# Performance work log

Hardware: AMD Instinct MI355X
Metric: run time of the kernel (lower is better)

The kernel has to match this reference:

```python
import jax, jax.numpy as jnp
import numpy as np

TAU = 1.0
EPS = 1e-8  # torch cosine_similarity norm clamp


def setup_inputs() -> dict:
    key = jax.random.key(0)
    k1, k2, k3 = jax.random.split(key, 3)
    B, d, M, C = 4096, 128, 8192, 16
    f = jax.random.normal(k1, (B, d), dtype=jnp.float32)
    f_neg = jax.random.normal(k2, (M, d), dtype=jnp.float32)
    labels = jax.random.randint(k3, (B,), 0, C, dtype=jnp.int64)
    return {"f": f, "f_neg": f_neg, "labels": labels, "batch_size": B}


def _normalize(x):
    n = jnp.linalg.norm(x, axis=-1, keepdims=True)
    return x / jnp.maximum(n, EPS)


def reference(f, f_neg, labels, batch_size):
    B = batch_size
    fn = _normalize(f)            # [B, d]
    gn = _normalize(f_neg)        # [M, d]

    sim_bb = jnp.einsum('id,jd->ij', fn, fn)   # [B, B] cosine sims in-batch
    sim_bn = jnp.einsum('id,md->im', fn, gn)   # [B, M] sims with neg bank

    offdiag = ~jnp.eye(B, dtype=bool)                       # exclude self
    pos_mask = (labels[:, None] == labels[None, :]) & offdiag  # [B, B]

    exp_bb = jnp.exp(sim_bb / TAU) * offdiag                # self row removed
    exp_bn = jnp.exp(sim_bn / TAU)
    # denominator_i = sum over all non-self in-batch + all bank negatives
    denom = exp_bb.sum(axis=1) + exp_bn.sum(axis=1)         # [B]

    # -log(exp(s_p/tau)/denom) = log(denom) - s_p/tau, averaged over positives
    neg_log = jnp.log(denom)[:, None] - sim_bb / TAU        # [B, B]
    n_pos = pos_mask.sum(axis=1)                            # [B]
    loss_i = jnp.sum(jnp.where(pos_mask, neg_log, 0.0), axis=1) / n_pos

    return jnp.sum(loss_i) / B  # reduction='mean'
```

## Files before the change

kernel.cpp:

```cpp
#include <hip/hip_runtime.h>
#include <hip/hip_bf16.h>
#include <hip/hip_fp8.h>

#define B_ROWS 4096
#define D_K    128
#define M_ROWS 8192
#define N_TOT  12288
#define NCHUNK 32
#define JT_PER_CHUNK 6
#define JCOLS  64
#define NCLS   16

typedef __attribute__((ext_vector_type(4))) int   intx4;
typedef __attribute__((ext_vector_type(8))) int   intx8;
typedef __attribute__((ext_vector_type(4))) float floatx4;

__device__ __forceinline__ float fp8_to_f32(unsigned char b) {
    __hip_fp8_e4m3 h; h.__x = b; return float(h);
}

__global__ __launch_bounds__(256) void nrm_kernel(
    const float* __restrict__ f, const float* __restrict__ fneg,
    unsigned char* __restrict__ G8, unsigned char* __restrict__ A8,
    float* __restrict__ S, int* __restrict__ hist, float* __restrict__ out)
{
    const int tid  = threadIdx.x;
    const int wave = tid >> 6;
    const int lane = tid & 63;
    const int row  = blockIdx.x * 4 + wave;
    if (blockIdx.x == 0) {
        #pragma unroll
        for (int k = 0; k < 8; ++k) S[tid + k * 256] = 0.f;
        if (tid < NCLS) hist[tid] = 0;
        if (tid == 0) out[0] = 0.f;
    }
    const float* src = (row < B_ROWS) ? (f + (size_t)row * D_K)
                                      : (fneg + (size_t)(row - B_ROWS) * D_K);
    float2 v = *reinterpret_cast<const float2*>(src + lane * 2);
    float ss = v.x * v.x + v.y * v.y;
    #pragma unroll
    for (int m = 1; m < 64; m <<= 1) ss += __shfl_xor(ss, m, 64);
    const float scale = 1.0f / fmaxf(sqrtf(ss), 1e-8f);
    __hip_fp8_e4m3 q0(v.x * scale);
    __hip_fp8_e4m3 q1(v.y * scale);
    const unsigned short pk =
        (unsigned short)q0.__x | ((unsigned short)q1.__x << 8);
    *reinterpret_cast<unsigned short*>(G8 + (size_t)row * D_K + lane * 2) = pk;
    if (row < B_ROWS) {
        const float s2 = scale * 1.44269504f;
        __hip_fp8_e4m3 a0(v.x * s2);
        __hip_fp8_e4m3 a1(v.y * s2);
        const unsigned short pa =
            (unsigned short)a0.__x | ((unsigned short)a1.__x << 8);
        *reinterpret_cast<unsigned short*>(A8 + (size_t)row * D_K + lane * 2) = pa;
    }
}

__global__ __launch_bounds__(256, 4) void sim_kernel(
    const unsigned char* __restrict__ G8, const unsigned char* __restrict__ A8,
    const int* __restrict__ labels, float* __restrict__ part_d,
    float* __restrict__ S, int* __restrict__ hist)
{
    __shared__ unsigned char Bs[2][JCOLS * D_K];

    const int tid = threadIdx.x;

    if (blockIdx.y >= 32) {
        const int svc    = (blockIdx.y - 32) * NCHUNK + blockIdx.x;
        const int stripe = svc & 31;
        const int dc     = svc >> 5;
        float* Sp = (float*)&Bs[0][0];
        int*   lh = (int*)(Sp + NCLS * 32);
        for (int k = tid; k < NCLS * 32; k += 256) Sp[k] = 0.f;
        if (tid < NCLS) lh[tid] = 0;
        __syncthreads();

        const int j0 = stripe * 128;
        if (dc == 0 && tid < 128) atomicAdd(&lh[labels[j0 + tid]], 1);

        const int d = tid & 31;
        const int w = tid >> 5;
        for (int jj = w; jj < 128; jj += 8) {
            const int j = j0 + jj;
            const int c = labels[j];
            atomicAdd(&Sp[c * 32 + d],
                      fp8_to_f32(G8[(size_t)j * D_K + dc * 32 + d]));
        }
        __syncthreads();
        for (int k = tid; k < NCLS * 32; k += 256)
            atomicAdd(&S[(k >> 5) * D_K + dc * 32 + (k & 31)], Sp[k]);
        if (dc == 0 && tid < NCLS) atomicAdd(&hist[tid], lh[tid]);
        return;
    }

    const int jc   = blockIdx.x;
    const int it   = blockIdx.y;
    const int wave = tid >> 6;
    const int lane = tid & 63;
    const int i0   = it * 128 + wave * 32;

    const int r16 = lane & 15;
    const int grp = lane >> 4;

    const unsigned char* Abase = A8 + (size_t)(i0 + r16) * D_K + grp * 32;
    intx8 afr[2];
    #pragma unroll
    for (int a = 0; a < 2; ++a)
        afr[a] = *reinterpret_cast<const intx8*>(Abase + (size_t)a * 16 * D_K);

    float dsum[2][4];
    #pragma unroll
    for (int a = 0; a < 2; ++a)
        #pragma unroll
        for (int r = 0; r < 4; ++r) dsum[a][r] = 0.f;

    int srcoff[2];
    #pragma unroll
    for (int s = 0; s < 2; ++s) {
        const int row  = s * 32 + (tid >> 3);
        const int gran = (tid & 7) ^ (row & 7);
        srcoff[s] = row * D_K + gran * 16;
    }

    intx4 streg[2];
    {
        const unsigned char* src =
            G8 + (size_t)(jc * JT_PER_CHUNK) * JCOLS * D_K;
        #pragma unroll
        for (int s = 0; s < 2; ++s)
            streg[s] = *reinterpret_cast<const intx4*>(src + srcoff[s]);
        #pragma unroll
        for (int s = 0; s < 2; ++s)
            *reinterpret_cast<intx4*>(&Bs[0][0] + s * 4096 + tid * 16) =
                streg[s];
    }

    for (int t = 0; t < JT_PER_CHUNK; ++t) {
        const int cur = t & 1;
        __syncthreads();

        if (t + 1 < JT_PER_CHUNK) {
            const unsigned char* src =
                G8 + (size_t)(jc * JT_PER_CHUNK + t + 1) * JCOLS * D_K;
            #pragma unroll
            for (int s = 0; s < 2; ++s)
                streg[s] = *reinterpret_cast<const intx4*>(src + srcoff[s]);
        }

        floatx4 acc[2][4];
        #pragma unroll
        for (int a = 0; a < 2; ++a)
            #pragma unroll
            for (int b = 0; b < 4; ++b)
                acc[a][b] = (floatx4){0.f, 0.f, 0.f, 0.f};

        const unsigned char* base = &Bs[cur][0];
        #pragma unroll
        for (int b = 0; b < 4; ++b) {
            const int jloc = b * 16 + r16;
            const int sw   = jloc & 7;
            intx4 lo = *reinterpret_cast<const intx4*>(
                base + jloc * D_K + ((2 * grp)     ^ sw) * 16);
            intx4 hi = *reinterpret_cast<const intx4*>(
                base + jloc * D_K + ((2 * grp + 1) ^ sw) * 16);
            intx8 bfr;
            #pragma unroll
            for (int e = 0; e < 4; ++e) { bfr[e] = lo[e]; bfr[e + 4] = hi[e]; }
            #pragma unroll
            for (int a = 0; a < 2; ++a)
                acc[a][b] = __builtin_amdgcn_mfma_scale_f32_16x16x128_f8f6f4(
                    afr[a], bfr, acc[a][b], 0, 0,
                    0, 0x7F7F7F7F, 0, 0x7F7F7F7F);
        }

        #pragma unroll
        for (int a = 0; a < 2; ++a)
            #pragma unroll
            for (int r = 0; r < 4; ++r) {
                float s0 = exp2f(acc[a][0][r]) + exp2f(acc[a][1][r]);
                float s1 = exp2f(acc[a][2][r]) + exp2f(acc[a][3][r]);
                dsum[a][r] += s0 + s1;
            }

        if (t + 1 < JT_PER_CHUNK) {
            #pragma unroll
            for (int s = 0; s < 2; ++s)
                *reinterpret_cast<intx4*>(
                    &Bs[cur ^ 1][0] + s * 4096 + tid * 16) = streg[s];
        }
    }

    #pragma unroll
    for (int a = 0; a < 2; ++a)
        #pragma unroll
        for (int r = 0; r < 4; ++r) {
            #pragma unroll
            for (int m = 1; m < 16; m <<= 1)
                dsum[a][r] += __shfl_xor(dsum[a][r], m, 64);
        }
    if (r16 == 0) {
        #pragma unroll
        for (int a = 0; a < 2; ++a)
            #pragma unroll
            for (int r = 0; r < 4; ++r)
                part_d[(size_t)(i0 + a * 16 + grp * 4 + r) * NCHUNK + jc] =
                    dsum[a][r];
    }
}

__global__ __launch_bounds__(256) void fin_kernel(
    const unsigned char* __restrict__ G8, const float* __restrict__ part_d,
    const float* __restrict__ S, const int* __restrict__ labels,
    const int* __restrict__ hist, float* __restrict__ out)
{
    const int tid  = threadIdx.x;
    const int wave = tid >> 6;
    const int lane = tid & 63;

    float lsum = 0.f;
    #pragma unroll 2
    for (int rr = 0; rr < 8; ++rr) {
        const int i   = (blockIdx.x * 4 + wave) * 8 + rr;
        const int lab = labels[i];
        float pd = (lane < NCHUNK) ? part_d[(size_t)i * NCHUNK + lane] : 0.f;
        const unsigned char* gr = G8 + (size_t)i * D_K + lane * 2;
        const float f0 = fp8_to_f32(gr[0]);
        const float f1 = fp8_to_f32(gr[1]);
        float2 sv = *reinterpret_cast<const float2*>(S + lab * D_K + lane * 2);
        float self = f0 * f0 + f1 * f1;
        float sp   = f0 * sv.x + f1 * sv.y;
        #pragma unroll
        for (int m = 1; m < 64; m <<= 1) {
            pd   += __shfl_xor(pd, m, 64);
            self += __shfl_xor(self, m, 64);
            sp   += __shfl_xor(sp, m, 64);
        }
        if (lane == 0) {
            const float npos  = (float)(hist[lab] - 1);
            const float denom = pd - __expf(self);
            lsum += __logf(denom) - (sp - self) / npos;
        }
    }
    __shared__ float w4[4];
    if (lane == 0) w4[wave] = lsum;
    __syncthreads();
    if (tid == 0)
        atomicAdd(out, (w4[0] + w4[1] + w4[2] + w4[3]) * (1.0f / (float)B_ROWS));
}

extern "C" void kernel_launch(void* const* d_in, const int* in_sizes, int n_in,
                              void* d_out, int out_size, void* d_ws, size_t ws_size,
                              hipStream_t stream) {
    const float* f      = (const float*)d_in[0];
    const float* fneg   = (const float*)d_in[1];
    const int*   labels = (const int*)d_in[2];
    float*       out    = (float*)d_out;

    char* ws = (char*)d_ws;
    unsigned char* G8     = (unsigned char*)(ws);
    unsigned char* A8     = (unsigned char*)(ws + 1572864);
    float*         part_d = (float*)(ws + 1572864 + 524288);
    float*         S      = (float*)(ws + 1572864 + 524288 + 524288);
    int*           hist   = (int*)(ws + 1572864 + 524288 + 524288 + 8192);

    nrm_kernel<<<N_TOT / 4, 256, 0, stream>>>(f, fneg, G8, A8, S, hist, out);

    dim3 gridS(NCHUNK, 36);
    sim_kernel<<<gridS, 256, 0, stream>>>(G8, A8, labels, part_d, S, hist);

    fin_kernel<<<128, 256, 0, stream>>>(G8, part_d, S, labels, hist, out);
}
```

Measured before the change: 36.17 us.

## Fuse finalize pass into sim kernel via global completion counters

Removes the separate finalize kernel launch. The 128 service blocks in the sim grid first build the class sums, then spin on global atomic counters until all 1024 sim blocks and all service blocks are done, and then compute the per-row loss themselves. This saves one launch and its gap. It risks deadlock if the spinning blocks occupy slots that the sim blocks still need, although the grid likely fits on the device. The spinning blocks also hold resources and add atomic traffic.

New measurement: 76.54 us. 112% more time.

```diff
diff --git a/kernel.cpp b/kernel.cpp
--- a/kernel.cpp
+++ b/kernel.cpp
@@ -10,6 +10,8 @@
 #define JT_PER_CHUNK 6
 #define JCOLS  64
 #define NCLS   16
+#define SIM_BLOCKS 1024
+#define SVC_BLOCKS 128
 
 typedef __attribute__((ext_vector_type(4))) int   intx4;
 typedef __attribute__((ext_vector_type(8))) int   intx8;
@@ -22,7 +24,8 @@
 __global__ __launch_bounds__(256) void nrm_kernel(
     const float* __restrict__ f, const float* __restrict__ fneg,
     unsigned char* __restrict__ G8, unsigned char* __restrict__ A8,
-    float* __restrict__ S, int* __restrict__ hist, float* __restrict__ out)
+    float* __restrict__ S, int* __restrict__ hist, float* __restrict__ out,
+    int* __restrict__ cnt)
 {
     const int tid  = threadIdx.x;
     const int wave = tid >> 6;
@@ -32,7 +35,7 @@
         #pragma unroll
         for (int k = 0; k < 8; ++k) S[tid + k * 256] = 0.f;
         if (tid < NCLS) hist[tid] = 0;
-        if (tid == 0) out[0] = 0.f;
+        if (tid == 0) { out[0] = 0.f; cnt[0] = 0; cnt[1] = 0; }
     }
     const float* src = (row < B_ROWS) ? (f + (size_t)row * D_K)
                                       : (fneg + (size_t)(row - B_ROWS) * D_K);
@@ -59,11 +62,14 @@
 __global__ __launch_bounds__(256, 4) void sim_kernel(
     const unsigned char* __restrict__ G8, const unsigned char* __restrict__ A8,
     const int* __restrict__ labels, float* __restrict__ part_d,
-    float* __restrict__ S, int* __restrict__ hist)
+    float* __restrict__ S, int* __restrict__ hist, float* __restrict__ out,
+    int* __restrict__ cnt)
 {
     __shared__ unsigned char Bs[2][JCOLS * D_K];
 
-    const int tid = threadIdx.x;
+    const int tid  = threadIdx.x;
+    const int wave = tid >> 6;
+    const int lane = tid & 63;
 
     if (blockIdx.y >= 32) {
         const int svc    = (blockIdx.y - 32) * NCHUNK + blockIdx.x;
@@ -90,14 +96,54 @@
         for (int k = tid; k < NCLS * 32; k += 256)
             atomicAdd(&S[(k >> 5) * D_K + dc * 32 + (k & 31)], Sp[k]);
         if (dc == 0 && tid < NCLS) atomicAdd(&hist[tid], lh[tid]);
+
+        __syncthreads();
+        if (tid == 0) {
+            __threadfence();
+            atomicAdd(&cnt[1], 1);
+            while (atomicAdd(&cnt[0], 0) < SIM_BLOCKS)
+                __builtin_amdgcn_s_sleep(8);
+            while (atomicAdd(&cnt[1], 0) < SVC_BLOCKS)
+                __builtin_amdgcn_s_sleep(8);
+            __threadfence();
+        }
+        __syncthreads();
+
+        float lsum = 0.f;
+        #pragma unroll 2
+        for (int rr = 0; rr < 8; ++rr) {
+            const int i   = (svc * 4 + wave) * 8 + rr;
+            const int lab = labels[i];
+            float pd = (lane < NCHUNK) ? part_d[(size_t)i * NCHUNK + lane] : 0.f;
+            const unsigned char* gr = G8 + (size_t)i * D_K + lane * 2;
+            const float f0 = fp8_to_f32(gr[0]);
+            const float f1 = fp8_to_f32(gr[1]);
+            float2 sv = *reinterpret_cast<const float2*>(S + lab * D_K + lane * 2);
+            float self = f0 * f0 + f1 * f1;
+            float sp   = f0 * sv.x + f1 * sv.y;
+            #pragma unroll
+            for (int m = 1; m < 64; m <<= 1) {
+                pd   += __shfl_xor(pd, m, 64);
+                self += __shfl_xor(self, m, 64);
+                sp   += __shfl_xor(sp, m, 64);
+            }
+            if (lane == 0) {
+                const float npos  = (float)(hist[lab] - 1);
+                const float denom = pd - __expf(self);
+                lsum += __logf(denom) - (sp - self) / npos;
+            }
+        }
+        __shared__ float w4[4];
+        if (lane == 0) w4[wave] = lsum;
+        __syncthreads();
+        if (tid == 0)
+            atomicAdd(out, (w4[0] + w4[1] + w4[2] + w4[3]) * (1.0f / (float)B_ROWS));
         return;
     }
 
-    const int jc   = blockIdx.x;
-    const int it   = blockIdx.y;
-    const int wave = tid >> 6;
-    const int lane = tid & 63;
-    const int i0   = it * 128 + wave * 32;
+    const int jc = blockIdx.x;
+    const int it = blockIdx.y;
+    const int i0 = it * 128 + wave * 32;
 
     const int r16 = lane & 15;
     const int grp = lane >> 4;
@@ -206,46 +252,12 @@
                 part_d[(size_t)(i0 + a * 16 + grp * 4 + r) * NCHUNK + jc] =
                     dsum[a][r];
     }
-}
-
-__global__ __launch_bounds__(256) void fin_kernel(
-    const unsigned char* __restrict__ G8, const float* __restrict__ part_d,
-    const float* __restrict__ S, const int* __restrict__ labels,
-    const int* __restrict__ hist, float* __restrict__ out)
-{
-    const int tid  = threadIdx.x;
-    const int wave = tid >> 6;
-    const int lane = tid & 63;
-
-    float lsum = 0.f;
-    #pragma unroll 2
-    for (int rr = 0; rr < 8; ++rr) {
-        const int i   = (blockIdx.x * 4 + wave) * 8 + rr;
-        const int lab = labels[i];
-        float pd = (lane < NCHUNK) ? part_d[(size_t)i * NCHUNK + lane] : 0.f;
-        const unsigned char* gr = G8 + (size_t)i * D_K + lane * 2;
-        const float f0 = fp8_to_f32(gr[0]);
-        const float f1 = fp8_to_f32(gr[1]);
-        float2 sv = *reinterpret_cast<const float2*>(S + lab * D_K + lane * 2);
-        float self = f0 * f0 + f1 * f1;
-        float sp   = f0 * sv.x + f1 * sv.y;
-        #pragma unroll
-        for (int m = 1; m < 64; m <<= 1) {
-            pd   += __shfl_xor(pd, m, 64);
-            self += __shfl_xor(self, m, 64);
-            sp   += __shfl_xor(sp, m, 64);
-        }
-        if (lane == 0) {
-            const float npos  = (float)(hist[lab] - 1);
-            const float denom = pd - __expf(self);
-            lsum += __logf(denom) - (sp - self) / npos;
-        }
-    }
-    __shared__ float w4[4];
-    if (lane == 0) w4[wave] = lsum;
+
     __syncthreads();
-    if (tid == 0)
-        atomicAdd(out, (w4[0] + w4[1] + w4[2] + w4[3]) * (1.0f / (float)B_ROWS));
+    if (tid == 0) {
+        __threadfence();
+        atomicAdd(&cnt[0], 1);
+    }
 }
 
 extern "C" void kernel_launch(void* const* d_in, const int* in_sizes, int n_in,
@@ -262,11 +274,10 @@
     float*         part_d = (float*)(ws + 1572864 + 524288);
     float*         S      = (float*)(ws + 1572864 + 524288 + 524288);
     int*           hist   = (int*)(ws + 1572864 + 524288 + 524288 + 8192);
-
-    nrm_kernel<<<N_TOT / 4, 256, 0, stream>>>(f, fneg, G8, A8, S, hist, out);
+    int*           cnt    = (int*)(ws + 1572864 + 524288 + 524288 + 8192 + 128);
+
+    nrm_kernel<<<N_TOT / 4, 256, 0, stream>>>(f, fneg, G8, A8, S, hist, out, cnt);
 
     dim3 gridS(NCHUNK, 36);
-    sim_kernel<<<gridS, 256, 0, stream>>>(G8, A8, labels, part_d, S, hist);
-
-    fin_kernel<<<128, 256, 0, stream>>>(G8, part_d, S, labels, hist, out);
-}
+    sim_kernel<<<gridS, 256, 0, stream>>>(G8, A8, labels, part_d, S, hist, out, cnt);
+}
```
